# Performance work log

Measured on AMD Instinct MI355X. Metric: run time of the kernel, lower is better.

## Reference

```python
import jax, jax.numpy as jnp
import numpy as np

D_MODEL = 256
N_HEAD = 8
HEAD_DIM = D_MODEL // N_HEAD
N_TOTAL = 24576
B, T = 64, 512


def setup_inputs() -> dict:
    key = jax.random.key(0)
    ks = jax.random.split(key, 12)
    s = 1.0 / np.sqrt(D_MODEL)
    return {
        "x": jax.random.normal(ks[0], (N_TOTAL, D_MODEL), jnp.float32),
        "Wq": jax.random.uniform(ks[1], (D_MODEL, D_MODEL), jnp.float32, -s, s),
        "bq": jax.random.uniform(ks[2], (D_MODEL,), jnp.float32, -s, s),
        "Wk": jax.random.uniform(ks[3], (D_MODEL, D_MODEL), jnp.float32, -s, s),
        "bk": jax.random.uniform(ks[4], (D_MODEL,), jnp.float32, -s, s),
        "Wv": jax.random.uniform(ks[5], (D_MODEL, D_MODEL), jnp.float32, -s, s),
        "bv": jax.random.uniform(ks[6], (D_MODEL,), jnp.float32, -s, s),
        "Wp": jax.random.uniform(ks[7], (D_MODEL, D_MODEL), jnp.float32, -s, s),
        "bp": jax.random.uniform(ks[8], (D_MODEL,), jnp.float32, -s, s),
        "padpack_index": jax.random.randint(ks[9], (B, T), 0, N_TOTAL, jnp.int64 if jax.config.jax_enable_x64 else jnp.int32),
        "padpack_batch": jax.random.randint(ks[10], (B, T), 0, B, jnp.int32),
        "padpack_inverse_index": jax.random.randint(ks[11], (N_TOTAL,), 0, B * T, jnp.int64 if jax.config.jax_enable_x64 else jnp.int32),
    }


def reference(x, Wq, bq, Wk, bk, Wv, bv, Wp, bp, padpack_index, padpack_batch, padpack_inverse_index):
    # gather ragged tokens into packed [B, T, C]
    xp = x[padpack_index]
    # mask: True where packed slots share the same segment id (matches
    # original masked_fill(batch_i == batch_j, -1e9))
    mask = padpack_batch[:, :, None] == padpack_batch[:, None, :]  # [B,T,T]
    # QKV projections (torch Linear: x @ W.T + b), split heads
    def heads(w, b):
        h = xp @ w.T + b
        return h.reshape(B, T, N_HEAD, HEAD_DIM).transpose(0, 2, 1, 3)  # [B,H,T,D]
    q, k, v = heads(Wq, bq), heads(Wk, bk), heads(Wv, bv)
    att = jnp.einsum("bhtd,bhsd->bhts", q, k) * (1.0 / np.sqrt(HEAD_DIM))
    att = jnp.where(mask[:, None], jnp.float32(-1e9), att)
    att = jax.nn.softmax(att, axis=-1)
    y = jnp.einsum("bhts,bhsd->bhtd", att, v)  # [B,H,T,D]
    y = y.transpose(0, 2, 1, 3).reshape(B, T, D_MODEL)
    y = y @ Wp.T + bp
    # scatter back to ragged layout
    return y.reshape(B * T, D_MODEL)[padpack_inverse_index]
```

## Files before the change

kernel.cpp:

```cpp
#include <hip/hip_runtime.h>


typedef __attribute__((ext_vector_type(8))) short short8;
typedef __attribute__((ext_vector_type(4))) float f32x4;

#define N_TOTAL 24576
#define B_ 64
#define T_ 512
#define DM 256
#define NH 8
#define HD 32
#define F3 768

#define QSCALE 0.25503463f
#define VSP 514

__device__ __forceinline__ unsigned short f2bf(float f) {
  unsigned int u = __float_as_uint(f);
  u += 0x7fffu + ((u >> 16) & 1u);
  return (unsigned short)(u >> 16);
}

__device__ __forceinline__ void gl_lds16(const void* g, void* l) {
  __builtin_amdgcn_global_load_lds(
      (const __attribute__((address_space(1))) unsigned int*)g,
      (__attribute__((address_space(3))) unsigned int*)l, 16, 0, 0);
}

__global__ __launch_bounds__(256) void pack_kernel(
    const float* __restrict__ x, const float* __restrict__ Wq,
    const float* __restrict__ Wk, const float* __restrict__ Wv,
    const float* __restrict__ Wp, const float* __restrict__ bq,
    const float* __restrict__ bk, const float* __restrict__ bv,
    const int* __restrict__ idx,
    short* __restrict__ XP, short* __restrict__ WCAT, short* __restrict__ WPb,
    float* __restrict__ BCAT) {
  int gid = blockIdx.x * 256 + threadIdx.x;
  if (gid < 768)
    BCAT[gid] = (gid < 256) ? bq[gid] : (gid < 512 ? bk[gid - 256] : bv[gid - 512]);
  const float* src;
  short* dst;
  if (gid < 1048576) {
    int row = gid >> 5, seg = gid & 31;
    src = x + (size_t)idx[row] * DM + seg * 8;
    dst = XP + (size_t)gid * 8;
  } else if (gid < 1073152) {
    int u = gid - 1048576;
    int f = u >> 5, seg = u & 31;
    const float* W = (f < 256) ? Wq : ((f < 512) ? Wk : Wv);
    src = W + (size_t)(f & 255) * DM + seg * 8;
    dst = WCAT + (size_t)u * 8;
  } else {
    int u = gid - 1073152;
    src = Wp + (size_t)u * 8;
    dst = WPb + (size_t)u * 8;
  }
  const float4* s4 = (const float4*)src;
  float4 a = s4[0], b = s4[1];
  short8 o;
  o[0] = (short)f2bf(a.x); o[1] = (short)f2bf(a.y);
  o[2] = (short)f2bf(a.z); o[3] = (short)f2bf(a.w);
  o[4] = (short)f2bf(b.x); o[5] = (short)f2bf(b.y);
  o[6] = (short)f2bf(b.z); o[7] = (short)f2bf(b.w);
  *(short8*)dst = o;
}

__global__ __launch_bounds__(256) void qkv_gemm(
    const short* __restrict__ XP, const short* __restrict__ WCAT,
    const float* __restrict__ BCAT, unsigned short* __restrict__ QKVp) {
  __shared__ __align__(16) char smem[3 * 16384];
  int tid = threadIdx.x;
  int lane = tid & 63, w = tid >> 6;
  int i = lane & 15, q = lane >> 4;
  int m0 = blockIdx.x * 128, n0 = blockIdx.y * 128;
  int wm = (w & 1) * 64, wn = (w >> 1) * 64;
  int csa = q ^ ((i >> 1) & 3);

  f32x4 zf = {0.f, 0.f, 0.f, 0.f};
  f32x4 acc[4][4];
#pragma unroll
  for (int mt = 0; mt < 4; mt++)
#pragma unroll
    for (int nt = 0; nt < 4; nt++) acc[mt][nt] = zf;

  auto stage = [&](int k, int s) {
#pragma unroll
    for (int p = 0; p < 2; p++) {
      int U = p * 256 + tid;
      int row = U >> 2, c = U & 3;
      int cs = c ^ ((row >> 1) & 3);
      gl_lds16(XP + (size_t)(m0 + row) * DM + k * 32 + cs * 8,
               smem + s * 16384 + U * 16);
      gl_lds16(WCAT + (size_t)(n0 + row) * DM + k * 32 + cs * 8,
               smem + s * 16384 + 8192 + U * 16);
    }
  };

  stage(0, 0);
  stage(1, 1);
#pragma unroll
  for (int k = 0; k < 8; k++) {
    if (k == 7)
      asm volatile("s_waitcnt vmcnt(0) lgkmcnt(0)\ns_barrier" ::: "memory");
    else
      asm volatile("s_waitcnt vmcnt(4) lgkmcnt(0)\ns_barrier" ::: "memory");
    const short* Asb = (const short*)(smem + (k % 3) * 16384);
    const short* Bsb = Asb + 4096;
    short8 a[4], bfr[4];
#pragma unroll
    for (int mt = 0; mt < 4; mt++)
      a[mt] = *(const short8*)&Asb[(wm + mt * 16 + i) * 32 + csa * 8];
#pragma unroll
    for (int nt = 0; nt < 4; nt++)
      bfr[nt] = *(const short8*)&Bsb[(wn + nt * 16 + i) * 32 + csa * 8];
    if (k < 6) stage(k + 2, (k + 2) % 3);
#pragma unroll
    for (int mt = 0; mt < 4; mt++)
#pragma unroll
      for (int nt = 0; nt < 4; nt++)
        acc[mt][nt] = __builtin_amdgcn_mfma_f32_16x16x32_bf16(a[mt], bfr[nt], acc[mt][nt], 0, 0, 0);
  }

  float scale = (n0 < 256) ? QSCALE : 1.0f;
#pragma unroll
  for (int nt = 0; nt < 4; nt++) {
    int f = n0 + wn + nt * 16 + i;
    float bias = BCAT[f];
#pragma unroll
    for (int mt = 0; mt < 4; mt++) {
#pragma unroll
      for (int r = 0; r < 4; r++) {
        int token = m0 + wm + mt * 16 + q * 4 + r;
        QKVp[(size_t)token * F3 + f] = f2bf((acc[mt][nt][r] + bias) * scale);
      }
    }
  }
}

__global__ __launch_bounds__(256) void attn_kernel(
    const unsigned short* __restrict__ QKVp, const int* __restrict__ batch,
    unsigned short* __restrict__ Y) {
  __shared__ __align__(16) short Vl[HD * VSP];
  __shared__ __align__(16) short pscr[4][64 * 40];
  __shared__ int sbat[T_];
  int tid = threadIdx.x, w = tid >> 6, lane = tid & 63;
  int i = lane & 15, q = lane >> 4;
  int bx = blockIdx.x;
  int half = bx >> 9, bh = bx & 511;
  int b = bh >> 3, h = bh & 7;
  int t0 = half * 256 + w * 64;
  const unsigned short* Tok = QKVp + (size_t)b * T_ * F3;

  *(int2*)&sbat[tid * 2] = *(const int2*)&batch[b * T_ + tid * 2];

  {
    int seg = tid & 3, sb = tid >> 2;
#pragma unroll
    for (int l = 0; l < 8; l++) {
      int s = sb + l * 64;
      short8 v = *(const short8*)&Tok[(size_t)s * F3 + 512 + h * HD + seg * 8];
#pragma unroll
      for (int j = 0; j < 8; j++) Vl[(seg * 8 + j) * VSP + s] = v[j];
    }
  }
  __syncthreads();

  short* pw = &pscr[w][0];

  short8 qf[4];
  int btv[4][4];
#pragma unroll
  for (int mt = 0; mt < 4; mt++)
    qf[mt] = *(const short8*)&Tok[(size_t)(t0 + mt * 16 + i) * F3 + h * HD + q * 8];
#pragma unroll
  for (int mt = 0; mt < 4; mt++) {
    int4 t4 = *(int4*)&sbat[t0 + mt * 16 + q * 4];
    btv[mt][0] = t4.x; btv[mt][1] = t4.y; btv[mt][2] = t4.z; btv[mt][3] = t4.w;
  }

  unsigned short ob = (i == 0) ? (unsigned short)0x3F80 : (unsigned short)0;
  short8 ones = {(short)ob, (short)ob, (short)ob, (short)ob,
                 (short)ob, (short)ob, (short)ob, (short)ob};

  f32x4 zf = {0.f, 0.f, 0.f, 0.f};
  f32x4 o[4][2], lacc[4];
#pragma unroll
  for (int mt = 0; mt < 4; mt++) {
    o[mt][0] = zf; o[mt][1] = zf; lacc[mt] = zf;
  }

  const unsigned short* Kcol = Tok + 256 + h * HD + q * 8;
  short8 k0f = *(const short8*)&Kcol[(size_t)(2 * i) * F3];
  short8 k1f = *(const short8*)&Kcol[(size_t)(2 * i + 1) * F3];
  int bs0 = sbat[2 * i], bs1 = sbat[2 * i + 1];

  for (int s0 = 0; s0 < T_; s0 += 32) {
    short8 ck0 = k0f, ck1 = k1f;
    int cb0 = bs0, cb1 = bs1;
    if (s0 + 32 < T_) {
      k0f = *(const short8*)&Kcol[(size_t)(s0 + 32 + 2 * i) * F3];
      k1f = *(const short8*)&Kcol[(size_t)(s0 + 32 + 2 * i + 1) * F3];
      bs0 = sbat[s0 + 32 + 2 * i];
      bs1 = sbat[s0 + 32 + 2 * i + 1];
    }
    short8 v0f = *(const short8*)&Vl[i * VSP + s0 + q * 8];
    short8 v1f = *(const short8*)&Vl[(16 + i) * VSP + s0 + q * 8];
#pragma unroll
    for (int mt = 0; mt < 4; mt++) {
      f32x4 st0 = __builtin_amdgcn_mfma_f32_16x16x32_bf16(qf[mt], ck0, zf, 0, 0, 0);
      f32x4 st1 = __builtin_amdgcn_mfma_f32_16x16x32_bf16(qf[mt], ck1, zf, 0, 0, 0);
#pragma unroll
      for (int r = 0; r < 4; r++) {
        float m0v = (btv[mt][r] == cb0) ? -1e9f : st0[r];
        float m1v = (btv[mt][r] == cb1) ? -1e9f : st1[r];
        unsigned e0 = __float_as_uint(__builtin_amdgcn_exp2f(m0v));
        unsigned e1 = __float_as_uint(__builtin_amdgcn_exp2f(m1v));
        unsigned pk = __builtin_amdgcn_perm(e1, e0, 0x07060302u);
        *(unsigned*)&pw[(mt * 16 + q * 4 + r) * 40 + 2 * i] = pk;
      }
    }
#pragma unroll
    for (int mt = 0; mt < 4; mt++) {
      short8 pa = *(short8*)&pw[(mt * 16 + i) * 40 + q * 8];
      o[mt][0] = __builtin_amdgcn_mfma_f32_16x16x32_bf16(pa, v0f, o[mt][0], 0, 0, 0);
      o[mt][1] = __builtin_amdgcn_mfma_f32_16x16x32_bf16(pa, v1f, o[mt][1], 0, 0, 0);
      lacc[mt] = __builtin_amdgcn_mfma_f32_16x16x32_bf16(pa, ones, lacc[mt], 0, 0, 0);
    }
  }

#pragma unroll
  for (int mt = 0; mt < 4; mt++) {
#pragma unroll
    for (int r = 0; r < 4; r++) {
      float lv = __shfl(lacc[mt][r], lane & 48, 64);
      float inv = __builtin_amdgcn_rcpf(lv);
      size_t yb = ((size_t)b * T_ + t0 + mt * 16 + q * 4 + r) * DM + h * HD;
      Y[yb + i] = f2bf(o[mt][0][r] * inv);
      Y[yb + 16 + i] = f2bf(o[mt][1][r] * inv);
    }
  }
}

__global__ __launch_bounds__(256) void out_gemm(
    const short* __restrict__ Y, const short* __restrict__ WPb,
    const float* __restrict__ bp, const int* __restrict__ inv,
    float* __restrict__ out) {
  __shared__ __align__(16) char smem[3 * 16384];
  int tid = threadIdx.x;
  int lane = tid & 63, w = tid >> 6;
  int i = lane & 15, q = lane >> 4;
  int m0 = blockIdx.x * 128, n0 = blockIdx.y * 128;
  int wm = (w & 1) * 64, wn = (w >> 1) * 64;
  int csa = q ^ ((i >> 1) & 3);

  int iv0 = inv[m0 + (tid >> 2)];
  int iv1 = inv[m0 + 64 + (tid >> 2)];

  f32x4 zf = {0.f, 0.f, 0.f, 0.f};
  f32x4 acc[4][4];
#pragma unroll
  for (int mt = 0; mt < 4; mt++)
#pragma unroll
    for (int nt = 0; nt < 4; nt++) acc[mt][nt] = zf;

  auto stage = [&](int k, int s) {
#pragma unroll
    for (int p = 0; p < 2; p++) {
      int U = p * 256 + tid;
      int row = U >> 2, c = U & 3;
      int cs = c ^ ((row >> 1) & 3);
      int iv = p ? iv1 : iv0;
      gl_lds16(Y + (size_t)iv * DM + k * 32 + cs * 8, smem + s * 16384 + U * 16);
      gl_lds16(WPb + (size_t)(n0 + row) * DM + k * 32 + cs * 8,
               smem + s * 16384 + 8192 + U * 16);
    }
  };

  stage(0, 0);
  stage(1, 1);
#pragma unroll
  for (int k = 0; k < 8; k++) {
    if (k == 7)
      asm volatile("s_waitcnt vmcnt(0) lgkmcnt(0)\ns_barrier" ::: "memory");
    else
      asm volatile("s_waitcnt vmcnt(4) lgkmcnt(0)\ns_barrier" ::: "memory");
    const short* Asb = (const short*)(smem + (k % 3) * 16384);
    const short* Bsb = Asb + 4096;
    short8 a[4], bfr[4];
#pragma unroll
    for (int mt = 0; mt < 4; mt++)
      a[mt] = *(const short8*)&Asb[(wm + mt * 16 + i) * 32 + csa * 8];
#pragma unroll
    for (int nt = 0; nt < 4; nt++)
      bfr[nt] = *(const short8*)&Bsb[(wn + nt * 16 + i) * 32 + csa * 8];
    if (k < 6) stage(k + 2, (k + 2) % 3);
#pragma unroll
    for (int mt = 0; mt < 4; mt++)
#pragma unroll
      for (int nt = 0; nt < 4; nt++)
        acc[mt][nt] = __builtin_amdgcn_mfma_f32_16x16x32_bf16(a[mt], bfr[nt], acc[mt][nt], 0, 0, 0);
  }

#pragma unroll
  for (int nt = 0; nt < 4; nt++) {
    int f = n0 + wn + nt * 16 + i;
    float bias = bp[f];
#pragma unroll
    for (int mt = 0; mt < 4; mt++) {
#pragma unroll
      for (int r = 0; r < 4; r++) {
        int row = m0 + wm + mt * 16 + q * 4 + r;
        out[(size_t)row * DM + f] = acc[mt][nt][r] + bias;
      }
    }
  }
}

extern "C" void kernel_launch(void* const* d_in, const int* in_sizes, int n_in,
                              void* d_out, int out_size, void* d_ws, size_t ws_size,
                              hipStream_t stream) {
  const float* x = (const float*)d_in[0];
  const float* Wq = (const float*)d_in[1];
  const float* bq = (const float*)d_in[2];
  const float* Wk = (const float*)d_in[3];
  const float* bk = (const float*)d_in[4];
  const float* Wv = (const float*)d_in[5];
  const float* bv = (const float*)d_in[6];
  const float* Wp = (const float*)d_in[7];
  const float* bp = (const float*)d_in[8];
  const int* idx = (const int*)d_in[9];
  const int* batch = (const int*)d_in[10];
  const int* inv = (const int*)d_in[11];
  float* out = (float*)d_out;

  char* ws = (char*)d_ws;
  short* XP = (short*)(ws + 0);
  short* WCAT = (short*)(ws + 16777216);
  short* WPb = (short*)(ws + 17170432);
  float* BCAT = (float*)(ws + 17301504);
  unsigned short* QKVp = (unsigned short*)(ws + 17304576);
  unsigned short* Yb = (unsigned short*)(ws + 67636224);

  pack_kernel<<<4224, 256, 0, stream>>>(x, Wq, Wk, Wv, Wp, bq, bk, bv, idx,
                                        XP, WCAT, WPb, BCAT);
  qkv_gemm<<<dim3(256, 6), 256, 0, stream>>>(XP, WCAT, BCAT, QKVp);
  attn_kernel<<<1024, 256, 0, stream>>>(QKVp, batch, Yb);
  out_gemm<<<dim3(192, 2), 256, 0, stream>>>((const short*)Yb, WPb, bp, inv, out);
}
```

Baseline: 180.1 us.

## Pre-transpose V into global buffer via separate kernel, read V directly in attention

Adds a vtrans_kernel that transposes each head's V slice into a [bh][d][t] global buffer, which reuses the XP workspace region after the QKV GEMM. The attention kernel drops its per-block LDS transpose of V and its large V shared buffer, and loads V fragments straight from global/L2. The block index mapping is also changed so the two halves of the same (b,h) run adjacently, improving L2 reuse of K/V. This removes duplicated V transposition across the two halves and lowers LDS use, which may raise occupancy. The cost is an extra kernel launch and an extra round trip of V through memory.

```diff
diff --git a/kernel.cpp b/kernel.cpp
--- a/kernel.cpp
+++ b/kernel.cpp
@@ -13,7 +13,7 @@
 #define F3 768
 
 #define QSCALE 0.25503463f
-#define VSP 514
+#define VSP 520
 
 __device__ __forceinline__ unsigned short f2bf(float f) {
   unsigned int u = __float_as_uint(f);
@@ -137,32 +137,47 @@
   }
 }
 
+__global__ __launch_bounds__(256) void vtrans_kernel(
+    const unsigned short* __restrict__ QKVp, unsigned short* __restrict__ Vt) {
+  __shared__ short Vl[HD * VSP];
+  int bh = blockIdx.x;
+  int b = bh >> 3, h = bh & 7;
+  int tid = threadIdx.x;
+  const unsigned short* src = QKVp + (size_t)b * T_ * F3 + 512 + h * HD;
+  int seg = tid & 3, trow = tid >> 2;
+#pragma unroll
+  for (int l = 0; l < 8; l++) {
+    int t = trow + l * 64;
+    short8 v = *(const short8*)&src[(size_t)t * F3 + seg * 8];
+#pragma unroll
+    for (int j = 0; j < 8; j++) Vl[(seg * 8 + j) * VSP + t] = v[j];
+  }
+  __syncthreads();
+  int d = tid >> 3, tc = tid & 7;
+#pragma unroll
+  for (int l = 0; l < 8; l++) {
+    int t = (tc + l * 8) * 8;
+    short8 v = *(const short8*)&Vl[d * VSP + t];
+    *(short8*)&Vt[((size_t)bh * HD + d) * T_ + t] = v;
+  }
+}
+
 __global__ __launch_bounds__(256) void attn_kernel(
-    const unsigned short* __restrict__ QKVp, const int* __restrict__ batch,
-    unsigned short* __restrict__ Y) {
-  __shared__ __align__(16) short Vl[HD * VSP];
+    const unsigned short* __restrict__ QKVp, const unsigned short* __restrict__ Vt,
+    const int* __restrict__ batch, unsigned short* __restrict__ Y) {
   __shared__ __align__(16) short pscr[4][64 * 40];
   __shared__ int sbat[T_];
   int tid = threadIdx.x, w = tid >> 6, lane = tid & 63;
   int i = lane & 15, q = lane >> 4;
   int bx = blockIdx.x;
-  int half = bx >> 9, bh = bx & 511;
+  int bh = ((bx >> 4) << 3) | (bx & 7);
+  int half = (bx >> 3) & 1;
   int b = bh >> 3, h = bh & 7;
   int t0 = half * 256 + w * 64;
   const unsigned short* Tok = QKVp + (size_t)b * T_ * F3;
+  const unsigned short* Vb = Vt + (size_t)bh * HD * T_;
 
   *(int2*)&sbat[tid * 2] = *(const int2*)&batch[b * T_ + tid * 2];
-
-  {
-    int seg = tid & 3, sb = tid >> 2;
-#pragma unroll
-    for (int l = 0; l < 8; l++) {
-      int s = sb + l * 64;
-      short8 v = *(const short8*)&Tok[(size_t)s * F3 + 512 + h * HD + seg * 8];
-#pragma unroll
-      for (int j = 0; j < 8; j++) Vl[(seg * 8 + j) * VSP + s] = v[j];
-    }
-  }
   __syncthreads();
 
   short* pw = &pscr[w][0];
@@ -203,8 +218,8 @@
       bs0 = sbat[s0 + 32 + 2 * i];
       bs1 = sbat[s0 + 32 + 2 * i + 1];
     }
-    short8 v0f = *(const short8*)&Vl[i * VSP + s0 + q * 8];
-    short8 v1f = *(const short8*)&Vl[(16 + i) * VSP + s0 + q * 8];
+    short8 v0f = *(const short8*)&Vb[(size_t)i * T_ + s0 + q * 8];
+    short8 v1f = *(const short8*)&Vb[(size_t)(16 + i) * T_ + s0 + q * 8];
 #pragma unroll
     for (int mt = 0; mt < 4; mt++) {
       f32x4 st0 = __builtin_amdgcn_mfma_f32_16x16x32_bf16(qf[mt], ck0, zf, 0, 0, 0);
@@ -340,10 +355,12 @@
   float* BCAT = (float*)(ws + 17301504);
   unsigned short* QKVp = (unsigned short*)(ws + 17304576);
   unsigned short* Yb = (unsigned short*)(ws + 67636224);
+  unsigned short* Vt = (unsigned short*)(ws + 0);
 
   pack_kernel<<<4224, 256, 0, stream>>>(x, Wq, Wk, Wv, Wp, bq, bk, bv, idx,
                                         XP, WCAT, WPb, BCAT);
   qkv_gemm<<<dim3(256, 6), 256, 0, stream>>>(XP, WCAT, BCAT, QKVp);
-  attn_kernel<<<1024, 256, 0, stream>>>(QKVp, batch, Yb);
+  vtrans_kernel<<<512, 256, 0, stream>>>(QKVp, Vt);
+  attn_kernel<<<1024, 256, 0, stream>>>(QKVp, Vt, batch, Yb);
   out_gemm<<<dim3(192, 2), 256, 0, stream>>>((const short*)Yb, WPb, bp, inv, out);
 }
```

New measurement: 186.3 us. 1.03x slower.

## Fuse gather+bf16 convert into QKV GEMM, emit transposed V, pipeline attention

Applied to the files above, without the earlier changes.

The x gather and fp32-to-bf16 conversion move out of the pack kernel and into the QKV GEMM, which loads fp32 rows straight into LDS by index and converts while building fragments. This removes the XP intermediate write and read. The GEMM epilogue for V blocks transposes through LDS and writes V in [b,h,d,t] layout, so the attention kernel no longer transposes V into LDS itself. The attention kernel double-buffers P in LDS and prefetches K/V one step ahead, overlapping the exp work with the PV MFMAs. The costs are a larger fp32 A tile in LDS and a truncation-style rounding of x instead of round-to-nearest-even.

```diff
diff --git a/kernel.cpp b/kernel.cpp
--- a/kernel.cpp
+++ b/kernel.cpp
@@ -10,10 +10,10 @@
 #define DM 256
 #define NH 8
 #define HD 32
-#define F3 768
+#define F2 512
 
 #define QSCALE 0.25503463f
-#define VSP 514
+#define PSTR 40
 
 __device__ __forceinline__ unsigned short f2bf(float f) {
   unsigned int u = __float_as_uint(f);
@@ -28,30 +28,23 @@
 }
 
 __global__ __launch_bounds__(256) void pack_kernel(
-    const float* __restrict__ x, const float* __restrict__ Wq,
-    const float* __restrict__ Wk, const float* __restrict__ Wv,
-    const float* __restrict__ Wp, const float* __restrict__ bq,
-    const float* __restrict__ bk, const float* __restrict__ bv,
-    const int* __restrict__ idx,
-    short* __restrict__ XP, short* __restrict__ WCAT, short* __restrict__ WPb,
-    float* __restrict__ BCAT) {
+    const float* __restrict__ Wq, const float* __restrict__ Wk,
+    const float* __restrict__ Wv, const float* __restrict__ Wp,
+    const float* __restrict__ bq, const float* __restrict__ bk,
+    const float* __restrict__ bv,
+    short* __restrict__ WCAT, short* __restrict__ WPb, float* __restrict__ BCAT) {
   int gid = blockIdx.x * 256 + threadIdx.x;
   if (gid < 768)
     BCAT[gid] = (gid < 256) ? bq[gid] : (gid < 512 ? bk[gid - 256] : bv[gid - 512]);
   const float* src;
   short* dst;
-  if (gid < 1048576) {
-    int row = gid >> 5, seg = gid & 31;
-    src = x + (size_t)idx[row] * DM + seg * 8;
-    dst = XP + (size_t)gid * 8;
-  } else if (gid < 1073152) {
-    int u = gid - 1048576;
-    int f = u >> 5, seg = u & 31;
+  if (gid < 24576) {
+    int f = gid >> 5, seg = gid & 31;
     const float* W = (f < 256) ? Wq : ((f < 512) ? Wk : Wv);
     src = W + (size_t)(f & 255) * DM + seg * 8;
-    dst = WCAT + (size_t)u * 8;
+    dst = WCAT + (size_t)gid * 8;
   } else {
-    int u = gid - 1073152;
+    int u = gid - 24576;
     src = Wp + (size_t)u * 8;
     dst = WPb + (size_t)u * 8;
   }
@@ -66,35 +59,45 @@
 }
 
 __global__ __launch_bounds__(256) void qkv_gemm(
-    const short* __restrict__ XP, const short* __restrict__ WCAT,
-    const float* __restrict__ BCAT, unsigned short* __restrict__ QKVp) {
-  __shared__ __align__(16) char smem[3 * 16384];
+    const float* __restrict__ x, const int* __restrict__ idx,
+    const short* __restrict__ WCAT, const float* __restrict__ BCAT,
+    unsigned short* __restrict__ QKp, unsigned short* __restrict__ Vt) {
+  __shared__ __align__(16) char smem[3 * 16384 + 3 * 8192];
   int tid = threadIdx.x;
   int lane = tid & 63, w = tid >> 6;
   int i = lane & 15, q = lane >> 4;
   int m0 = blockIdx.x * 128, n0 = blockIdx.y * 128;
   int wm = (w & 1) * 64, wn = (w >> 1) * 64;
-  int csa = q ^ ((i >> 1) & 3);
-
-  f32x4 zf = {0.f, 0.f, 0.f, 0.f};
-  f32x4 acc[4][4];
-#pragma unroll
-  for (int mt = 0; mt < 4; mt++)
-#pragma unroll
-    for (int nt = 0; nt < 4; nt++) acc[mt][nt] = zf;
+  int csb = q ^ ((i >> 1) & 3);
+  char* smB = smem + 3 * 16384;
+
+  int ivp[4];
+#pragma unroll
+  for (int p = 0; p < 4; p++) ivp[p] = idx[m0 + p * 32 + (tid >> 3)];
 
   auto stage = [&](int k, int s) {
+#pragma unroll
+    for (int p = 0; p < 4; p++) {
+      int U = p * 256 + tid;
+      int cg = (U & 7) ^ ((tid >> 3) & 7);
+      gl_lds16(x + (size_t)ivp[p] * DM + k * 32 + cg * 4, smem + s * 16384 + U * 16);
+    }
 #pragma unroll
     for (int p = 0; p < 2; p++) {
       int U = p * 256 + tid;
       int row = U >> 2, c = U & 3;
       int cs = c ^ ((row >> 1) & 3);
-      gl_lds16(XP + (size_t)(m0 + row) * DM + k * 32 + cs * 8,
-               smem + s * 16384 + U * 16);
       gl_lds16(WCAT + (size_t)(n0 + row) * DM + k * 32 + cs * 8,
-               smem + s * 16384 + 8192 + U * 16);
+               smB + s * 8192 + U * 16);
     }
   };
+
+  f32x4 zf = {0.f, 0.f, 0.f, 0.f};
+  f32x4 acc[4][4];
+#pragma unroll
+  for (int mt = 0; mt < 4; mt++)
+#pragma unroll
+    for (int nt = 0; nt < 4; nt++) acc[mt][nt] = zf;
 
   stage(0, 0);
   stage(1, 1);
@@ -103,16 +106,30 @@
     if (k == 7)
       asm volatile("s_waitcnt vmcnt(0) lgkmcnt(0)\ns_barrier" ::: "memory");
     else
-      asm volatile("s_waitcnt vmcnt(4) lgkmcnt(0)\ns_barrier" ::: "memory");
-    const short* Asb = (const short*)(smem + (k % 3) * 16384);
-    const short* Bsb = Asb + 4096;
+      asm volatile("s_waitcnt vmcnt(6) lgkmcnt(0)\ns_barrier" ::: "memory");
+    const float* Asb = (const float*)(smem + (k % 3) * 16384);
+    const short* Bsb = (const short*)(smB + (k % 3) * 8192);
     short8 a[4], bfr[4];
 #pragma unroll
-    for (int mt = 0; mt < 4; mt++)
-      a[mt] = *(const short8*)&Asb[(wm + mt * 16 + i) * 32 + csa * 8];
+    for (int mt = 0; mt < 4; mt++) {
+      int m = wm + mt * 16 + i;
+      int s0 = (2 * q) ^ (i & 7), s1 = (2 * q + 1) ^ (i & 7);
+      f32x4 lo = *(const f32x4*)&Asb[m * 32 + s0 * 4];
+      f32x4 hi = *(const f32x4*)&Asb[m * 32 + s1 * 4];
+      unsigned u0 = __float_as_uint(lo[0]) + 0x8000u, u1 = __float_as_uint(lo[1]) + 0x8000u;
+      unsigned u2 = __float_as_uint(lo[2]) + 0x8000u, u3 = __float_as_uint(lo[3]) + 0x8000u;
+      unsigned u4 = __float_as_uint(hi[0]) + 0x8000u, u5 = __float_as_uint(hi[1]) + 0x8000u;
+      unsigned u6 = __float_as_uint(hi[2]) + 0x8000u, u7 = __float_as_uint(hi[3]) + 0x8000u;
+      unsigned pk0 = __builtin_amdgcn_perm(u1, u0, 0x07060302u);
+      unsigned pk1 = __builtin_amdgcn_perm(u3, u2, 0x07060302u);
+      unsigned pk2 = __builtin_amdgcn_perm(u5, u4, 0x07060302u);
+      unsigned pk3 = __builtin_amdgcn_perm(u7, u6, 0x07060302u);
+      unsigned pks[4] = {pk0, pk1, pk2, pk3};
+      a[mt] = *(short8*)pks;
+    }
 #pragma unroll
     for (int nt = 0; nt < 4; nt++)
-      bfr[nt] = *(const short8*)&Bsb[(wn + nt * 16 + i) * 32 + csa * 8];
+      bfr[nt] = *(const short8*)&Bsb[(wn + nt * 16 + i) * 32 + csb * 8];
     if (k < 6) stage(k + 2, (k + 2) % 3);
 #pragma unroll
     for (int mt = 0; mt < 4; mt++)
@@ -121,57 +138,75 @@
         acc[mt][nt] = __builtin_amdgcn_mfma_f32_16x16x32_bf16(a[mt], bfr[nt], acc[mt][nt], 0, 0, 0);
   }
 
-  float scale = (n0 < 256) ? QSCALE : 1.0f;
-#pragma unroll
-  for (int nt = 0; nt < 4; nt++) {
-    int f = n0 + wn + nt * 16 + i;
-    float bias = BCAT[f];
-#pragma unroll
-    for (int mt = 0; mt < 4; mt++) {
-#pragma unroll
-      for (int r = 0; r < 4; r++) {
-        int token = m0 + wm + mt * 16 + q * 4 + r;
-        QKVp[(size_t)token * F3 + f] = f2bf((acc[mt][nt][r] + bias) * scale);
+  if (blockIdx.y < 4) {
+    float scale = (n0 < 256) ? QSCALE : 1.0f;
+#pragma unroll
+    for (int nt = 0; nt < 4; nt++) {
+      int f = n0 + wn + nt * 16 + i;
+      float bias = BCAT[f];
+#pragma unroll
+      for (int mt = 0; mt < 4; mt++) {
+#pragma unroll
+        for (int r = 0; r < 4; r++) {
+          int token = m0 + wm + mt * 16 + q * 4 + r;
+          QKp[(size_t)token * F2 + f] = f2bf((acc[mt][nt][r] + bias) * scale);
+        }
       }
     }
+  } else {
+    int vb = blockIdx.y - 4;
+    short* TT = (short*)smem;
+    __syncthreads();
+#pragma unroll
+    for (int nt = 0; nt < 4; nt++) {
+      int fl = wn + nt * 16 + i;
+      float bias = BCAT[512 + vb * 128 + fl];
+#pragma unroll
+      for (int mt = 0; mt < 4; mt++) {
+#pragma unroll
+        for (int r = 0; r < 4; r++) {
+          int ml = wm + mt * 16 + q * 4 + r;
+          TT[fl * 136 + ml] = (short)f2bf(acc[mt][nt][r] + bias);
+        }
+      }
+    }
+    __syncthreads();
+    int fl = tid >> 1, half = tid & 1;
+    int fg = vb * 128 + fl;
+    int hh = fg >> 5, dd = fg & 31;
+    int bb = m0 >> 9, tt0 = m0 & 511;
+    unsigned short* dstrow = Vt + ((size_t)(bb * NH + hh) * HD + dd) * T_ + tt0 + half * 64;
+#pragma unroll
+    for (int j = 0; j < 8; j++) {
+      short8 v = *(const short8*)&TT[fl * 136 + half * 64 + j * 8];
+      *(short8*)&dstrow[j * 8] = v;
+    }
   }
 }
 
 __global__ __launch_bounds__(256) void attn_kernel(
-    const unsigned short* __restrict__ QKVp, const int* __restrict__ batch,
-    unsigned short* __restrict__ Y) {
-  __shared__ __align__(16) short Vl[HD * VSP];
-  __shared__ __align__(16) short pscr[4][64 * 40];
+    const unsigned short* __restrict__ QKp, const unsigned short* __restrict__ Vt,
+    const int* __restrict__ batch, unsigned short* __restrict__ Y) {
+  __shared__ __align__(16) short pscr[4][2][64 * PSTR];
   __shared__ int sbat[T_];
   int tid = threadIdx.x, w = tid >> 6, lane = tid & 63;
   int i = lane & 15, q = lane >> 4;
   int bx = blockIdx.x;
-  int half = bx >> 9, bh = bx & 511;
+  int bh = ((bx >> 4) << 3) | (bx & 7);
+  int half = (bx >> 3) & 1;
   int b = bh >> 3, h = bh & 7;
   int t0 = half * 256 + w * 64;
-  const unsigned short* Tok = QKVp + (size_t)b * T_ * F3;
+  const unsigned short* Tok = QKp + (size_t)b * T_ * F2;
+  const unsigned short* Vb = Vt + (size_t)bh * HD * T_;
 
   *(int2*)&sbat[tid * 2] = *(const int2*)&batch[b * T_ + tid * 2];
-
-  {
-    int seg = tid & 3, sb = tid >> 2;
-#pragma unroll
-    for (int l = 0; l < 8; l++) {
-      int s = sb + l * 64;
-      short8 v = *(const short8*)&Tok[(size_t)s * F3 + 512 + h * HD + seg * 8];
-#pragma unroll
-      for (int j = 0; j < 8; j++) Vl[(seg * 8 + j) * VSP + s] = v[j];
-    }
-  }
   __syncthreads();
-
-  short* pw = &pscr[w][0];
 
   short8 qf[4];
   int btv[4][4];
 #pragma unroll
   for (int mt = 0; mt < 4; mt++)
-    qf[mt] = *(const short8*)&Tok[(size_t)(t0 + mt * 16 + i) * F3 + h * HD + q * 8];
+    qf[mt] = *(const short8*)&Tok[(size_t)(t0 + mt * 16 + i) * F2 + h * HD + q * 8];
 #pragma unroll
   for (int mt = 0; mt < 4; mt++) {
     int4 t4 = *(int4*)&sbat[t0 + mt * 16 + q * 4];
@@ -190,41 +225,68 @@
   }
 
   const unsigned short* Kcol = Tok + 256 + h * HD + q * 8;
-  short8 k0f = *(const short8*)&Kcol[(size_t)(2 * i) * F3];
-  short8 k1f = *(const short8*)&Kcol[(size_t)(2 * i + 1) * F3];
-  int bs0 = sbat[2 * i], bs1 = sbat[2 * i + 1];
-
-  for (int s0 = 0; s0 < T_; s0 += 32) {
-    short8 ck0 = k0f, ck1 = k1f;
-    int cb0 = bs0, cb1 = bs1;
-    if (s0 + 32 < T_) {
-      k0f = *(const short8*)&Kcol[(size_t)(s0 + 32 + 2 * i) * F3];
-      k1f = *(const short8*)&Kcol[(size_t)(s0 + 32 + 2 * i + 1) * F3];
-      bs0 = sbat[s0 + 32 + 2 * i];
-      bs1 = sbat[s0 + 32 + 2 * i + 1];
-    }
-    short8 v0f = *(const short8*)&Vl[i * VSP + s0 + q * 8];
-    short8 v1f = *(const short8*)&Vl[(16 + i) * VSP + s0 + q * 8];
+
+  auto computeP = [&](int buf, short8 ka, short8 kb, int ba, int bb2) {
+    short* pw = &pscr[w][buf][0];
 #pragma unroll
     for (int mt = 0; mt < 4; mt++) {
-      f32x4 st0 = __builtin_amdgcn_mfma_f32_16x16x32_bf16(qf[mt], ck0, zf, 0, 0, 0);
-      f32x4 st1 = __builtin_amdgcn_mfma_f32_16x16x32_bf16(qf[mt], ck1, zf, 0, 0, 0);
+      f32x4 st0 = __builtin_amdgcn_mfma_f32_16x16x32_bf16(qf[mt], ka, zf, 0, 0, 0);
+      f32x4 st1 = __builtin_amdgcn_mfma_f32_16x16x32_bf16(qf[mt], kb, zf, 0, 0, 0);
 #pragma unroll
       for (int r = 0; r < 4; r++) {
-        float m0v = (btv[mt][r] == cb0) ? -1e9f : st0[r];
-        float m1v = (btv[mt][r] == cb1) ? -1e9f : st1[r];
+        float m0v = (btv[mt][r] == ba) ? -1e9f : st0[r];
+        float m1v = (btv[mt][r] == bb2) ? -1e9f : st1[r];
         unsigned e0 = __float_as_uint(__builtin_amdgcn_exp2f(m0v));
         unsigned e1 = __float_as_uint(__builtin_amdgcn_exp2f(m1v));
         unsigned pk = __builtin_amdgcn_perm(e1, e0, 0x07060302u);
-        *(unsigned*)&pw[(mt * 16 + q * 4 + r) * 40 + 2 * i] = pk;
+        *(unsigned*)&pw[(mt * 16 + q * 4 + r) * PSTR + 2 * i] = pk;
       }
     }
+  };
+
+  short8 kn0, kn1, vc0, vc1, vn0, vn1;
+  int bn0, bn1;
+  {
+    short8 ka = *(const short8*)&Kcol[(size_t)(2 * i) * F2];
+    short8 kb = *(const short8*)&Kcol[(size_t)(2 * i + 1) * F2];
+    int ba = sbat[2 * i], bb2 = sbat[2 * i + 1];
+    computeP(0, ka, kb, ba, bb2);
+  }
+  vc0 = *(const short8*)&Vb[(size_t)i * T_ + q * 8];
+  vc1 = *(const short8*)&Vb[(size_t)(16 + i) * T_ + q * 8];
+  kn0 = *(const short8*)&Kcol[(size_t)(32 + 2 * i) * F2];
+  kn1 = *(const short8*)&Kcol[(size_t)(32 + 2 * i + 1) * F2];
+  bn0 = sbat[32 + 2 * i]; bn1 = sbat[32 + 2 * i + 1];
+  vn0 = *(const short8*)&Vb[(size_t)i * T_ + 32 + q * 8];
+  vn1 = *(const short8*)&Vb[(size_t)(16 + i) * T_ + 32 + q * 8];
+
+  for (int it = 0; it < 16; it++) {
+    int cur = it & 1;
+    short* pr = &pscr[w][cur][0];
+    short8 pa[4];
+#pragma unroll
+    for (int mt = 0; mt < 4; mt++)
+      pa[mt] = *(short8*)&pr[(mt * 16 + i) * PSTR + q * 8];
+    if (it < 15) {
+      computeP(1 - cur, kn0, kn1, bn0, bn1);
+      if (it < 14) {
+        int s2 = (it + 2) * 32;
+        kn0 = *(const short8*)&Kcol[(size_t)(s2 + 2 * i) * F2];
+        kn1 = *(const short8*)&Kcol[(size_t)(s2 + 2 * i + 1) * F2];
+        bn0 = sbat[s2 + 2 * i]; bn1 = sbat[s2 + 2 * i + 1];
+      }
+    }
 #pragma unroll
     for (int mt = 0; mt < 4; mt++) {
-      short8 pa = *(short8*)&pw[(mt * 16 + i) * 40 + q * 8];
-      o[mt][0] = __builtin_amdgcn_mfma_f32_16x16x32_bf16(pa, v0f, o[mt][0], 0, 0, 0);
-      o[mt][1] = __builtin_amdgcn_mfma_f32_16x16x32_bf16(pa, v1f, o[mt][1], 0, 0, 0);
-      lacc[mt] = __builtin_amdgcn_mfma_f32_16x16x32_bf16(pa, ones, lacc[mt], 0, 0, 0);
+      o[mt][0] = __builtin_amdgcn_mfma_f32_16x16x32_bf16(pa[mt], vc0, o[mt][0], 0, 0, 0);
+      o[mt][1] = __builtin_amdgcn_mfma_f32_16x16x32_bf16(pa[mt], vc1, o[mt][1], 0, 0, 0);
+      lacc[mt] = __builtin_amdgcn_mfma_f32_16x16x32_bf16(pa[mt], ones, lacc[mt], 0, 0, 0);
+    }
+    vc0 = vn0; vc1 = vn1;
+    if (it < 14) {
+      int s2 = (it + 2) * 32;
+      vn0 = *(const short8*)&Vb[(size_t)i * T_ + s2 + q * 8];
+      vn1 = *(const short8*)&Vb[(size_t)(16 + i) * T_ + s2 + q * 8];
     }
   }
 
@@ -334,16 +396,16 @@
   float* out = (float*)d_out;
 
   char* ws = (char*)d_ws;
-  short* XP = (short*)(ws + 0);
-  short* WCAT = (short*)(ws + 16777216);
-  short* WPb = (short*)(ws + 17170432);
-  float* BCAT = (float*)(ws + 17301504);
-  unsigned short* QKVp = (unsigned short*)(ws + 17304576);
-  unsigned short* Yb = (unsigned short*)(ws + 67636224);
-
-  pack_kernel<<<4224, 256, 0, stream>>>(x, Wq, Wk, Wv, Wp, bq, bk, bv, idx,
-                                        XP, WCAT, WPb, BCAT);
-  qkv_gemm<<<dim3(256, 6), 256, 0, stream>>>(XP, WCAT, BCAT, QKVp);
-  attn_kernel<<<1024, 256, 0, stream>>>(QKVp, batch, Yb);
+  short* WCAT = (short*)(ws + 0);
+  short* WPb = (short*)(ws + 393216);
+  float* BCAT = (float*)(ws + 524288);
+  unsigned short* QKp = (unsigned short*)(ws + 1048576);
+  unsigned short* Vt = (unsigned short*)(ws + 34603008);
+  unsigned short* Yb = (unsigned short*)(ws + 51380224);
+
+  pack_kernel<<<128, 256, 0, stream>>>(Wq, Wk, Wv, Wp, bq, bk, bv,
+                                       WCAT, WPb, BCAT);
+  qkv_gemm<<<dim3(256, 6), 256, 0, stream>>>(x, idx, WCAT, BCAT, QKp, Vt);
+  attn_kernel<<<1024, 256, 0, stream>>>(QKp, Vt, batch, Yb);
   out_gemm<<<dim3(192, 2), 256, 0, stream>>>((const short*)Yb, WPb, bp, inv, out);
 }
```

Measured after the change: 181.6 us. Within noise of the previous version (+0.8%).
